# Performance work log

Hardware: AMD Instinct MI355X
Metric: run time of the kernel (lower is better)

## Reference

```python
import jax, jax.numpy as jnp
import numpy as np

N_NODES = 50000
N_EDGES = 800000
F_IN = 128
HID = 64
HEADS = 4
CLASSES = 40
NEG_SLOPE = 0.2
EPS = 1e-16


def glorot(key, shape):
    fan_in, fan_out = shape[0], shape[-1]
    lim = jnp.sqrt(6.0 / (fan_in + fan_out))
    return jax.random.uniform(key, shape, jnp.float32, -lim, lim)


def setup_inputs() -> dict:
    key = jax.random.key(0)
    ks = jax.random.split(key, 10)
    x = jax.random.normal(ks[0], (N_NODES, F_IN), jnp.float32)
    edge_index = jax.random.randint(ks[1], (2, N_EDGES), 0, N_NODES, jnp.int64)
    # layer 1: F_IN -> HID per head, HEADS heads, concat
    W1 = glorot(ks[2], (F_IN, HEADS * HID))
    a_src1 = glorot(ks[3], (1, HEADS, HID))
    a_dst1 = glorot(ks[4], (1, HEADS, HID))
    b1 = jnp.zeros((HEADS * HID,), jnp.float32)
    # layer 2: HEADS*HID -> CLASSES, 1 head
    W2 = glorot(ks[5], (HEADS * HID, CLASSES))
    a_src2 = glorot(ks[6], (1, 1, CLASSES))
    a_dst2 = glorot(ks[7], (1, 1, CLASSES))
    b2 = jnp.zeros((CLASSES,), jnp.float32)
    return {"x": x, "edge_index": edge_index, "W1": W1, "a_src1": a_src1,
            "a_dst1": a_dst1, "b1": b1, "W2": W2, "a_src2": a_src2,
            "a_dst2": a_dst2, "b2": b2}


def gat_conv(x, src, dst, W, a_src, a_dst, bias, heads, out_dim):
    n = x.shape[0]
    h = (x @ W).reshape(n, heads, out_dim)           # [N,H,D]
    alpha_s = jnp.sum(h * a_src, axis=-1)            # [N,H]
    alpha_d = jnp.sum(h * a_dst, axis=-1)            # [N,H]
    e = alpha_s[src] + alpha_d[dst]                  # [E,H]
    e = jax.nn.leaky_relu(e, NEG_SLOPE)
    # segment softmax over edges grouped by destination node
    m = jax.ops.segment_max(e, dst, num_segments=n)  # [N,H]
    ex = jnp.exp(e - m[dst])
    denom = jax.ops.segment_sum(ex, dst, num_segments=n)
    alpha = ex / (denom[dst] + EPS)                  # [E,H]
    msg = h[src] * alpha[:, :, None]                 # [E,H,D]
    out = jax.ops.segment_sum(msg, dst, num_segments=n)
    return out.reshape(n, heads * out_dim) + bias


def reference(x, edge_index, W1, a_src1, a_dst1, b1, W2, a_src2, a_dst2, b2):
    src, dst = edge_index[0], edge_index[1]
    h = gat_conv(x, src, dst, W1, a_src1, a_dst1, b1, HEADS, HID)
    h = jax.nn.relu(h)
    h = gat_conv(h, src, dst, W2, a_src2, a_dst2, b2, 1, CLASSES)
    return jax.nn.log_softmax(h, axis=1)
```

## Files before the change

### kernel.cpp

```cpp
#include <hip/hip_runtime.h>
#include <math.h>

#define NN 50000
#define NE 800000
#define FIN 128
#define HID 64
#define HEADS 4
#define C1 256
#define CLS 40
#define EPSF 1e-16f

#define NB 98
#define BSH 9
#define BSTRIDE 9216
#define NBLK_B 625
#define CHUNK 1280

typedef __attribute__((ext_vector_type(8))) short bf16x8;
typedef __attribute__((ext_vector_type(4))) float f32x4;
typedef __attribute__((ext_vector_type(2))) float f32x2;

__device__ __forceinline__ unsigned short f2bf(float f) {
    unsigned int u = __float_as_uint(f);
    unsigned int r = (u + 0x7fffu + ((u >> 16) & 1u)) >> 16;
    return (unsigned short)r;
}
__device__ __forceinline__ float bflo(unsigned int u) { return __uint_as_float(u << 16); }
__device__ __forceinline__ float bfhi(unsigned int u) { return __uint_as_float(u & 0xffff0000u); }
__device__ __forceinline__ unsigned char f2fp8(float v) {
    int pk = __builtin_amdgcn_cvt_pk_fp8_f32(v, v, 0, false);
    return (unsigned char)(pk & 0xff);
}
__device__ __forceinline__ float lrelu(float e) { return e > 0.f ? e : 0.2f * e; }

__global__ __launch_bounds__(512) void k_bucket(const int* __restrict__ ei,
                                                int* __restrict__ gcur,
                                                unsigned int* __restrict__ stage) {
    __shared__ unsigned int lchunk[CHUNK];
    __shared__ unsigned int lsort[CHUNK];
    __shared__ int lhist[128];
    __shared__ int sbuf[128];
    __shared__ int lstart[128];
    __shared__ int lbase[128];
    __shared__ int lcur[128];
    int t = threadIdx.x;
    int e0 = blockIdx.x * CHUNK;
    if (t < 128) lhist[t] = 0;
    __syncthreads();
    for (int j = t; j < CHUNK; j += 512) {
        int s = ei[e0 + j];
        int d = ei[NE + e0 + j];
        int b = d >> BSH;
        atomicAdd(&lhist[b], 1);
        lchunk[j] = (unsigned int)s | ((unsigned int)(d & 511) << 16) |
                    ((unsigned int)b << 25);
    }
    __syncthreads();
    if (t < 128) sbuf[t] = lhist[t];
    __syncthreads();
    for (int d = 1; d < 128; d <<= 1) {
        int x = (t < 128 && t >= d) ? sbuf[t - d] : 0;
        __syncthreads();
        if (t < 128) sbuf[t] += x;
        __syncthreads();
    }
    if (t < 128) {
        int excl = sbuf[t] - lhist[t];
        lstart[t] = excl;
        lcur[t] = excl;
        if (t < NB) lbase[t] = atomicAdd(&gcur[t], lhist[t]);
    }
    __syncthreads();
    for (int j = t; j < CHUNK; j += 512) {
        unsigned int pk = lchunk[j];
        int b = pk >> 25;
        int pos = atomicAdd(&lcur[b], 1);
        lsort[pos] = pk;
    }
    __syncthreads();
    for (int j = t; j < CHUNK; j += 512) {
        unsigned int pk = lsort[j];
        int b = pk >> 25;
        int dest = lbase[b] + (j - lstart[b]);
        stage[(size_t)b * BSTRIDE + dest] = pk & 0x01FFFFFFu;
    }
}

__global__ void k_bscan(const int* __restrict__ gcur, int* __restrict__ gbase) {
    __shared__ int s[128];
    int t = threadIdx.x;
    int v = (t < NB) ? gcur[t] : 0;
    s[t] = v;
    __syncthreads();
    for (int d = 1; d < 128; d <<= 1) {
        int x = (t >= d) ? s[t - d] : 0;
        __syncthreads();
        s[t] += x;
        __syncthreads();
    }
    if (t < NB) gbase[t] = s[t] - v;
}

__global__ __launch_bounds__(512) void k_bsort(const unsigned int* __restrict__ stage,
                                               const int* __restrict__ gcur,
                                               const int* __restrict__ gbase_a,
                                               int* __restrict__ offs,
                                               int* __restrict__ ssrc) {
    __shared__ int lhist[512];
    __shared__ int cur[512];
    int t = threadIdx.x;
    int b = blockIdx.x;
    int cnt = gcur[b];
    int gbase = gbase_a[b];
    const unsigned int* sp = stage + (size_t)b * BSTRIDE;
    lhist[t] = 0;
    __syncthreads();
    for (int j = t; j < cnt; j += 512) atomicAdd(&lhist[(sp[j] >> 16) & 511], 1);
    __syncthreads();
    if (t < 64) {
        int base = t * 8;
        int vals[8];
        int run = 0;
#pragma unroll
        for (int j = 0; j < 8; j++) { int v = lhist[base + j]; vals[j] = run; run += v; }
        int sc = run;
#pragma unroll
        for (int d = 1; d < 64; d <<= 1) { int u = __shfl_up(sc, d); if (t >= d) sc += u; }
        int excl = sc - run;
#pragma unroll
        for (int j = 0; j < 8; j++) cur[base + j] = excl + vals[j];
    }
    __syncthreads();
    offs[(b << BSH) + t] = gbase + cur[t];
    __syncthreads();
    for (int j = t; j < cnt; j += 512) {
        unsigned int v = sp[j];
        int dl = (v >> 16) & 511;
        int pos = atomicAdd(&cur[dl], 1);
        ssrc[gbase + pos] = (int)(v & 0xFFFFu);
    }
}

__global__ __launch_bounds__(256) void k_wconv(const float* __restrict__ W1,
                                               const float* __restrict__ W2,
                                               unsigned short* __restrict__ wB1,
                                               unsigned short* __restrict__ wB2) {
    int t = blockIdx.x * 256 + threadIdx.x;
    if (t < 4096) {
        int tn = t >> 8;
        int kc = (t >> 6) & 3;
        int l = t & 63;
        int n = tn * 16 + (l & 15);
        int k0 = kc * 32 + (l >> 4) * 8;
        unsigned short* o = wB1 + (size_t)t * 8;
#pragma unroll
        for (int j = 0; j < 8; j++) o[j] = f2bf(W1[(size_t)(k0 + j) * C1 + n]);
    } else if (t < 4096 + 1536) {
        int u = t - 4096;
        int tn = u >> 9;
        int kc = (u >> 6) & 7;
        int l = u & 63;
        int n = tn * 16 + (l & 15);
        int k0 = kc * 32 + (l >> 4) * 8;
        unsigned short* o = wB2 + (size_t)u * 8;
#pragma unroll
        for (int j = 0; j < 8; j++)
            o[j] = (n < CLS) ? f2bf(W2[(size_t)(k0 + j) * CLS + n]) : (unsigned short)0;
    }
}

__global__ __launch_bounds__(256) void k_gemm1(const float* __restrict__ x,
                                               const unsigned short* __restrict__ wB,
                                               const float* __restrict__ aws,
                                               const float* __restrict__ awd,
                                               unsigned char* __restrict__ h1f8,
                                               float* __restrict__ as1,
                                               float* __restrict__ ad1) {
    __shared__ uint4 Af[4][4][64];
    int t = threadIdx.x;
    int m0 = blockIdx.x * 64;
    int l = t & 63;
    int wv = t >> 6;

    bf16x8 bf[4][4];
    const bf16x8* wb = (const bf16x8*)wB + l;
#pragma unroll
    for (int tn = 0; tn < 4; tn++)
#pragma unroll
        for (int kc = 0; kc < 4; kc++)
            bf[tn][kc] = wb[(((wv * 4 + tn) * 4 + kc)) * 64];

#pragma unroll
    for (int i = 0; i < 8; i++) {
        int g = i * 256 + t;
        int row = g >> 5;
        int c4 = g & 31;
        int grow = m0 + row;
        if (grow >= NN) grow = NN - 1;
        float4 v = *(const float4*)(x + (size_t)grow * FIN + c4 * 4);
        uint2 pk;
        pk.x = (unsigned int)f2bf(v.x) | ((unsigned int)f2bf(v.y) << 16);
        pk.y = (unsigned int)f2bf(v.z) | ((unsigned int)f2bf(v.w) << 16);
        int kc = c4 >> 3;
        int rem = (c4 & 7) * 4;
        int q = rem >> 3;
        int hh = (rem >> 2) & 1;
        int ll = q * 16 + (row & 15);
        int mt = row >> 4;
        ((uint2*)&Af[mt][kc][ll])[hh] = pk;
    }
    __syncthreads();

    int q = l >> 4;
    int c = l & 15;

#pragma unroll
    for (int mt = 0; mt < 4; mt++) {
        bf16x8 a[4];
#pragma unroll
        for (int kc = 0; kc < 4; kc++) a[kc] = *(const bf16x8*)&Af[mt][kc][l];

        f32x4 acc[4];
#pragma unroll
        for (int tn = 0; tn < 4; tn++) acc[tn] = (f32x4){0.f, 0.f, 0.f, 0.f};
#pragma unroll
        for (int tn = 0; tn < 4; tn++) {
            acc[tn] = __builtin_amdgcn_mfma_f32_16x16x32_bf16(a[0], bf[tn][0], acc[tn], 0, 0, 0);
            acc[tn] = __builtin_amdgcn_mfma_f32_16x16x32_bf16(a[1], bf[tn][1], acc[tn], 0, 0, 0);
            acc[tn] = __builtin_amdgcn_mfma_f32_16x16x32_bf16(a[2], bf[tn][2], acc[tn], 0, 0, 0);
            acc[tn] = __builtin_amdgcn_mfma_f32_16x16x32_bf16(a[3], bf[tn][3], acc[tn], 0, 0, 0);
        }

        int row0 = m0 + mt * 16 + q * 4;
        float ps[4] = {0.f, 0.f, 0.f, 0.f}, pd[4] = {0.f, 0.f, 0.f, 0.f};
#pragma unroll
        for (int tn = 0; tn < 4; tn++) {
            int col = wv * 64 + tn * 16 + c;
            float wsv = aws[col];
            float wdv = awd[col];
#pragma unroll
            for (int r = 0; r < 4; r++) {
                float v = acc[tn][r];
                int row = row0 + r;
                if (row < NN) h1f8[(size_t)row * C1 + col] = f2fp8(v);
                ps[r] = fmaf(v, wsv, ps[r]);
                pd[r] = fmaf(v, wdv, pd[r]);
            }
        }
#pragma unroll
        for (int r = 0; r < 4; r++) {
            float a_ = ps[r], d_ = pd[r];
#pragma unroll
            for (int s = 1; s < 16; s <<= 1) {
                a_ += __shfl_xor(a_, s);
                d_ += __shfl_xor(d_, s);
            }
            int row = row0 + r;
            if (c == 0 && row < NN) {
                as1[row * 4 + wv] = a_;
                ad1[row * 4 + wv] = d_;
            }
        }
    }
}

__global__ __launch_bounds__(256) void k_agg1(const unsigned char* __restrict__ h1f8,
                                              const float* __restrict__ as1,
                                              const float* __restrict__ ad1,
                                              const int* __restrict__ offs,
                                              const int* __restrict__ ssrc,
                                              const float* __restrict__ b1,
                                              unsigned short* __restrict__ g1b) {
    int lane = threadIdx.x & 63;
    int half = lane >> 5;
    int hl = lane & 31;
    int head = hl >> 3;
    int node = blockIdx.x * 4 + (threadIdx.x >> 6);
    int beg = offs[node];
    int end = (node + 1 < NN) ? offs[node + 1] : NE;
    float adv = ad1[node * 4 + head];
    float l = 0.f;
    float acc[8];
#pragma unroll
    for (int c = 0; c < 8; c++) acc[c] = 0.f;
    const uint2* hv = (const uint2*)h1f8;

    if (beg < end) {
        int idx[4];
#pragma unroll
        for (int i = 0; i < 4; i++) idx[i] = ssrc[beg + 2 * i + half];
        uint2 hbA[2];
        float pA[2];
#pragma unroll
        for (int i = 0; i < 2; i++) {
            hbA[i] = hv[(size_t)idx[i] * 32 + hl];
            int e = beg + 2 * i + half;
            float p = __expf(lrelu(as1[idx[i] * 4 + head] + adv));
            pA[i] = (e < end) ? p : 0.f;
        }
        for (int j = beg; j < end; j += 8) {
            int idxN[4];
#pragma unroll
            for (int i = 0; i < 4; i++) idxN[i] = ssrc[j + 8 + 2 * i + half];
            uint2 hbB[2];
            float pB[2];
#pragma unroll
            for (int i = 0; i < 2; i++) {
                hbB[i] = hv[(size_t)idx[2 + i] * 32 + hl];
                int e = j + 4 + 2 * i + half;
                float p = __expf(lrelu(as1[idx[2 + i] * 4 + head] + adv));
                pB[i] = (e < end) ? p : 0.f;
            }
#pragma unroll
            for (int i = 0; i < 2; i++) {
                float p = pA[i];
                f32x2 v0 = __builtin_amdgcn_cvt_pk_f32_fp8(hbA[i].x, false);
                f32x2 v1 = __builtin_amdgcn_cvt_pk_f32_fp8(hbA[i].x, true);
                f32x2 v2 = __builtin_amdgcn_cvt_pk_f32_fp8(hbA[i].y, false);
                f32x2 v3 = __builtin_amdgcn_cvt_pk_f32_fp8(hbA[i].y, true);
                l += p;
                acc[0] = fmaf(p, v0.x, acc[0]);
                acc[1] = fmaf(p, v0.y, acc[1]);
                acc[2] = fmaf(p, v1.x, acc[2]);
                acc[3] = fmaf(p, v1.y, acc[3]);
                acc[4] = fmaf(p, v2.x, acc[4]);
                acc[5] = fmaf(p, v2.y, acc[5]);
                acc[6] = fmaf(p, v3.x, acc[6]);
                acc[7] = fmaf(p, v3.y, acc[7]);
            }
#pragma unroll
            for (int i = 0; i < 2; i++) {
                hbA[i] = hv[(size_t)idxN[i] * 32 + hl];
                int e = j + 8 + 2 * i + half;
                float p = __expf(lrelu(as1[idxN[i] * 4 + head] + adv));
                pA[i] = (e < end) ? p : 0.f;
            }
#pragma unroll
            for (int i = 0; i < 2; i++) {
                float p = pB[i];
                f32x2 v0 = __builtin_amdgcn_cvt_pk_f32_fp8(hbB[i].x, false);
                f32x2 v1 = __builtin_amdgcn_cvt_pk_f32_fp8(hbB[i].x, true);
                f32x2 v2 = __builtin_amdgcn_cvt_pk_f32_fp8(hbB[i].y, false);
                f32x2 v3 = __builtin_amdgcn_cvt_pk_f32_fp8(hbB[i].y, true);
                l += p;
                acc[0] = fmaf(p, v0.x, acc[0]);
                acc[1] = fmaf(p, v0.y, acc[1]);
                acc[2] = fmaf(p, v1.x, acc[2]);
                acc[3] = fmaf(p, v1.y, acc[3]);
                acc[4] = fmaf(p, v2.x, acc[4]);
                acc[5] = fmaf(p, v2.y, acc[5]);
                acc[6] = fmaf(p, v3.x, acc[6]);
                acc[7] = fmaf(p, v3.y, acc[7]);
            }
#pragma unroll
            for (int i = 0; i < 4; i++) idx[i] = idxN[i];
        }
    }
    l += __shfl_xor(l, 32);
#pragma unroll
    for (int c = 0; c < 8; c++) acc[c] += __shfl_xor(acc[c], 32);

    if (half == 0) {
        float inv = 1.f / (l + EPSF);
        const float4* b1v = (const float4*)b1;
        float4 b0 = b1v[hl * 2];
        float4 b1_ = b1v[hl * 2 + 1];
        float o[8];
        o[0] = fmaxf(fmaf(acc[0], inv, b0.x), 0.f);
        o[1] = fmaxf(fmaf(acc[1], inv, b0.y), 0.f);
        o[2] = fmaxf(fmaf(acc[2], inv, b0.z), 0.f);
        o[3] = fmaxf(fmaf(acc[3], inv, b0.w), 0.f);
        o[4] = fmaxf(fmaf(acc[4], inv, b1_.x), 0.f);
        o[5] = fmaxf(fmaf(acc[5], inv, b1_.y), 0.f);
        o[6] = fmaxf(fmaf(acc[6], inv, b1_.z), 0.f);
        o[7] = fmaxf(fmaf(acc[7], inv, b1_.w), 0.f);
        uint4 ob;
        ob.x = (unsigned int)f2bf(o[0]) | ((unsigned int)f2bf(o[1]) << 16);
        ob.y = (unsigned int)f2bf(o[2]) | ((unsigned int)f2bf(o[3]) << 16);
        ob.z = (unsigned int)f2bf(o[4]) | ((unsigned int)f2bf(o[5]) << 16);
        ob.w = (unsigned int)f2bf(o[6]) | ((unsigned int)f2bf(o[7]) << 16);
        ((uint4*)g1b)[(size_t)node * 32 + hl] = ob;
    }
}

__global__ __launch_bounds__(256) void k_gemm2(const unsigned short* __restrict__ g1b,
                                               const unsigned short* __restrict__ wB2,
                                               const float* __restrict__ aws,
                                               const float* __restrict__ awd,
                                               unsigned short* __restrict__ h2b,
                                               float* __restrict__ as2,
                                               float* __restrict__ ad2) {
    __shared__ uint4 Af[4][8][64];
    int t = threadIdx.x;
    int m0 = blockIdx.x * 64;

#pragma unroll
    for (int i = 0; i < 8; i++) {
        int g = i * 256 + t;
        int row = g >> 5;
        int c8 = g & 31;
        int grow = m0 + row;
        if (grow >= NN) grow = NN - 1;
        uint4 v = *(const uint4*)(g1b + (size_t)grow * C1 + c8 * 8);
        int kc = c8 >> 2;
        int q = c8 & 3;
        Af[row >> 4][kc][q * 16 + (row & 15)] = v;
    }
    __syncthreads();

    int l = t & 63;
    int wv = t >> 6;

    bf16x8 a[8];
#pragma unroll
    for (int kc = 0; kc < 8; kc++) a[kc] = *(const bf16x8*)&Af[wv][kc][l];

    f32x4 acc[3];
#pragma unroll
    for (int tn = 0; tn < 3; tn++) acc[tn] = (f32x4){0.f, 0.f, 0.f, 0.f};

    const bf16x8* wb = (const bf16x8*)wB2 + l;
#pragma unroll
    for (int tn = 0; tn < 3; tn++) {
#pragma unroll
        for (int kc = 0; kc < 8; kc++) {
            bf16x8 b = wb[(tn * 8 + kc) * 64];
            acc[tn] = __builtin_amdgcn_mfma_f32_16x16x32_bf16(a[kc], b, acc[tn], 0, 0, 0);
        }
    }

    int q = l >> 4;
    int c = l & 15;
    int row0 = m0 + wv * 16 + q * 4;
    float ps[4] = {0.f, 0.f, 0.f, 0.f}, pd[4] = {0.f, 0.f, 0.f, 0.f};
#pragma unroll
    for (int tn = 0; tn < 3; tn++) {
        int col = tn * 16 + c;
        bool cok = col < CLS;
        float wsv = cok ? aws[col] : 0.f;
        float wdv = cok ? awd[col] : 0.f;
#pragma unroll
        for (int r = 0; r < 4; r++) {
            float v = acc[tn][r];
            int row = row0 + r;
            if (cok && row < NN) h2b[(size_t)row * CLS + col] = f2bf(v);
            ps[r] = fmaf(v, wsv, ps[r]);
            pd[r] = fmaf(v, wdv, pd[r]);
        }
    }
#pragma unroll
    for (int r = 0; r < 4; r++) {
        float a_ = ps[r], d_ = pd[r];
#pragma unroll
        for (int s = 1; s < 16; s <<= 1) {
            a_ += __shfl_xor(a_, s);
            d_ += __shfl_xor(d_, s);
        }
        int row = row0 + r;
        if (c == 0 && row < NN) {
            as2[row] = a_;
            ad2[row] = d_;
        }
    }
}

__global__ __launch_bounds__(256) void k_agg2(const unsigned short* __restrict__ h2b,
                                              const float* __restrict__ as2,
                                              const float* __restrict__ ad2,
                                              const int* __restrict__ offs,
                                              const int* __restrict__ ssrc,
                                              const float* __restrict__ b2,
                                              float* __restrict__ out) {
    int lane = threadIdx.x & 63;
    int half = lane >> 5;
    int hl = lane & 31;
    int cl = hl < 20 ? hl : 19;
    int node = blockIdx.x * 4 + (threadIdx.x >> 6);
    int beg = offs[node];
    int end = (node + 1 < NN) ? offs[node + 1] : NE;
    float adv = ad2[node];
    float l = 0.f, aL = 0.f, aH = 0.f;
    const unsigned int* hv = (const unsigned int*)h2b;

    if (beg < end) {
        int idx[4];
#pragma unroll
        for (int i = 0; i < 4; i++) idx[i] = ssrc[beg + 2 * i + half];
        unsigned int hbA[2];
        float pA[2];
#pragma unroll
        for (int i = 0; i < 2; i++) {
            hbA[i] = hv[(size_t)idx[i] * 20 + cl];
            int e = beg + 2 * i + half;
            float p = __expf(lrelu(as2[idx[i]] + adv));
            pA[i] = (e < end) ? p : 0.f;
        }
        for (int j = beg; j < end; j += 8) {
            int idxN[4];
#pragma unroll
            for (int i = 0; i < 4; i++) idxN[i] = ssrc[j + 8 + 2 * i + half];
            unsigned int hbB[2];
            float pB[2];
#pragma unroll
            for (int i = 0; i < 2; i++) {
                hbB[i] = hv[(size_t)idx[2 + i] * 20 + cl];
                int e = j + 4 + 2 * i + half;
                float p = __expf(lrelu(as2[idx[2 + i]] + adv));
                pB[i] = (e < end) ? p : 0.f;
            }
#pragma unroll
            for (int i = 0; i < 2; i++) {
                float p = pA[i];
                l += p;
                aL = fmaf(p, bflo(hbA[i]), aL);
                aH = fmaf(p, bfhi(hbA[i]), aH);
            }
#pragma unroll
            for (int i = 0; i < 2; i++) {
                hbA[i] = hv[(size_t)idxN[i] * 20 + cl];
                int e = j + 8 + 2 * i + half;
                float p = __expf(lrelu(as2[idxN[i]] + adv));
                pA[i] = (e < end) ? p : 0.f;
            }
#pragma unroll
            for (int i = 0; i < 2; i++) {
                float p = pB[i];
                l += p;
                aL = fmaf(p, bflo(hbB[i]), aL);
                aH = fmaf(p, bfhi(hbB[i]), aH);
            }
#pragma unroll
            for (int i = 0; i < 4; i++) idx[i] = idxN[i];
        }
    }
    l += __shfl_xor(l, 32);
    aL += __shfl_xor(aL, 32);
    aH += __shfl_xor(aH, 32);

    if (half == 0) {
        bool act = hl < 20;
        float inv = 1.f / (l + EPSF);
        float vL = -INFINITY, vH = -INFINITY;
        if (act) {
            float2 b = ((const float2*)b2)[cl];
            vL = aL * inv + b.x;
            vH = aH * inv + b.y;
        }
        float mx = fmaxf(vL, vH);
#pragma unroll
        for (int s = 16; s >= 1; s >>= 1) mx = fmaxf(mx, __shfl_xor(mx, s));
        float ex = act ? (__expf(vL - mx) + __expf(vH - mx)) : 0.f;
#pragma unroll
        for (int s = 16; s >= 1; s >>= 1) ex += __shfl_xor(ex, s);
        if (act) {
            float ls = __logf(ex);
            float2 o = {vL - mx - ls, vH - mx - ls};
            *(float2*)(out + (size_t)node * CLS + cl * 2) = o;
        }
    }
}


extern "C" void kernel_launch(void* const* d_in, const int* in_sizes, int n_in,
                              void* d_out, int out_size, void* d_ws, size_t ws_size,
                              hipStream_t stream) {
    const float* x    = (const float*)d_in[0];
    const int*   ei   = (const int*)d_in[1];
    const float* W1   = (const float*)d_in[2];
    const float* as1w = (const float*)d_in[3];
    const float* ad1w = (const float*)d_in[4];
    const float* b1   = (const float*)d_in[5];
    const float* W2   = (const float*)d_in[6];
    const float* as2w = (const float*)d_in[7];
    const float* ad2w = (const float*)d_in[8];
    const float* b2   = (const float*)d_in[9];
    float* out = (float*)d_out;

    char* p = (char*)d_ws;
    auto alloc = [&](size_t bytes) {
        char* r = p;
        p += (bytes + 255) & ~(size_t)255;
        return r;
    };
    unsigned char* h1f8 = (unsigned char*)alloc((size_t)NN * C1);
    unsigned short* g1b = (unsigned short*)alloc((size_t)NN * C1 * 2);
    unsigned short* h2b = (unsigned short*)alloc((size_t)NN * CLS * 2);
    float* as1  = (float*)alloc((size_t)NN * 4 * 4);
    float* ad1  = (float*)alloc((size_t)NN * 4 * 4);
    float* as2  = (float*)alloc((size_t)NN * 4);
    float* ad2  = (float*)alloc((size_t)NN * 4);
    int* offs   = (int*)alloc((size_t)(NN + 1024) * 4);
    int* gcur   = (int*)alloc(128 * 4);
    int* gbase  = (int*)alloc(128 * 4);
    unsigned int* stage = (unsigned int*)alloc((size_t)NB * BSTRIDE * 4);
    int* ssrc   = (int*)alloc((size_t)(NE + 64) * 4);
    unsigned short* wB1 = (unsigned short*)alloc((size_t)4096 * 8 * 2);
    unsigned short* wB2 = (unsigned short*)alloc((size_t)1536 * 8 * 2);

    hipMemsetAsync(gcur, 0, 128 * 4, stream);
    hipMemsetAsync(ssrc + NE, 0, 64 * 4, stream);

    k_bucket<<<NBLK_B, 512, 0, stream>>>(ei, gcur, stage);
    k_bscan<<<1, 128, 0, stream>>>(gcur, gbase);
    k_bsort<<<NB, 512, 0, stream>>>(stage, gcur, gbase, offs, ssrc);

    k_wconv<<<22, 256, 0, stream>>>(W1, W2, wB1, wB2);
    k_gemm1<<<(NN + 63) / 64, 256, 0, stream>>>(x, wB1, as1w, ad1w, h1f8, as1, ad1);
    k_agg1<<<NN / 4, 256, 0, stream>>>(h1f8, as1, ad1, offs, ssrc, b1, g1b);

    k_gemm2<<<(NN + 63) / 64, 256, 0, stream>>>(g1b, wB2, as2w, ad2w, h2b, as2, ad2);
    k_agg2<<<NN / 4, 256, 0, stream>>>(h2b, as2, ad2, offs, ssrc, b2, out);
}
```

Before: 215.4 us.

## Fold weight conversion and bucket scan into sort kernels; widen aggregation lanes

Weight bf16 conversion is merged into the first 11 blocks of the bucketing kernel, and the bucket prefix scan is recomputed inside each bsort block. Together these remove two small kernel launches. Both aggregation kernels now split each wavefront into 4 edge groups of 16 lanes, with wider per-lane loads (16 fp8 or 4 bf16 values), so each wavefront has more edges in flight. The cost is more accumulator registers, an extra cross-lane reduction step, and more wasted masked loads on low-degree nodes.

```diff
diff --git a/kernel.cpp b/kernel.cpp
--- a/kernel.cpp
+++ b/kernel.cpp
@@ -35,7 +35,11 @@
 
 __global__ __launch_bounds__(512) void k_bucket(const int* __restrict__ ei,
                                                 int* __restrict__ gcur,
-                                                unsigned int* __restrict__ stage) {
+                                                unsigned int* __restrict__ stage,
+                                                const float* __restrict__ W1,
+                                                const float* __restrict__ W2,
+                                                unsigned short* __restrict__ wB1,
+                                                unsigned short* __restrict__ wB2) {
     __shared__ unsigned int lchunk[CHUNK];
     __shared__ unsigned int lsort[CHUNK];
     __shared__ int lhist[128];
@@ -44,6 +48,32 @@
     __shared__ int lbase[128];
     __shared__ int lcur[128];
     int t = threadIdx.x;
+
+    if (blockIdx.x < 11) {
+        int tw = blockIdx.x * 512 + t;
+        if (tw < 4096) {
+            int tn = tw >> 8;
+            int kc = (tw >> 6) & 3;
+            int lw = tw & 63;
+            int n = tn * 16 + (lw & 15);
+            int k0 = kc * 32 + (lw >> 4) * 8;
+            unsigned short* o = wB1 + (size_t)tw * 8;
+#pragma unroll
+            for (int j = 0; j < 8; j++) o[j] = f2bf(W1[(size_t)(k0 + j) * C1 + n]);
+        } else if (tw < 4096 + 1536) {
+            int u = tw - 4096;
+            int tn = u >> 9;
+            int kc = (u >> 6) & 7;
+            int lw = u & 63;
+            int n = tn * 16 + (lw & 15);
+            int k0 = kc * 32 + (lw >> 4) * 8;
+            unsigned short* o = wB2 + (size_t)u * 8;
+#pragma unroll
+            for (int j = 0; j < 8; j++)
+                o[j] = (n < CLS) ? f2bf(W2[(size_t)(k0 + j) * CLS + n]) : (unsigned short)0;
+        }
+    }
+
     int e0 = blockIdx.x * CHUNK;
     if (t < 128) lhist[t] = 0;
     __syncthreads();
@@ -86,35 +116,27 @@
     }
 }
 
-__global__ void k_bscan(const int* __restrict__ gcur, int* __restrict__ gbase) {
-    __shared__ int s[128];
-    int t = threadIdx.x;
-    int v = (t < NB) ? gcur[t] : 0;
-    s[t] = v;
-    __syncthreads();
-    for (int d = 1; d < 128; d <<= 1) {
-        int x = (t >= d) ? s[t - d] : 0;
-        __syncthreads();
-        s[t] += x;
-        __syncthreads();
-    }
-    if (t < NB) gbase[t] = s[t] - v;
-}
-
 __global__ __launch_bounds__(512) void k_bsort(const unsigned int* __restrict__ stage,
                                                const int* __restrict__ gcur,
-                                               const int* __restrict__ gbase_a,
                                                int* __restrict__ offs,
                                                int* __restrict__ ssrc) {
     __shared__ int lhist[512];
     __shared__ int cur[512];
+    __shared__ int sbuf[128];
     int t = threadIdx.x;
     int b = blockIdx.x;
     int cnt = gcur[b];
-    int gbase = gbase_a[b];
     const unsigned int* sp = stage + (size_t)b * BSTRIDE;
+    if (t < 128) sbuf[t] = (t < NB) ? gcur[t] : 0;
     lhist[t] = 0;
     __syncthreads();
+    for (int d = 1; d < 128; d <<= 1) {
+        int x = (t < 128 && t >= d) ? sbuf[t - d] : 0;
+        __syncthreads();
+        if (t < 128) sbuf[t] += x;
+        __syncthreads();
+    }
+    int gbase = sbuf[b] - cnt;
     for (int j = t; j < cnt; j += 512) atomicAdd(&lhist[(sp[j] >> 16) & 511], 1);
     __syncthreads();
     if (t < 64) {
@@ -138,34 +160,6 @@
         int dl = (v >> 16) & 511;
         int pos = atomicAdd(&cur[dl], 1);
         ssrc[gbase + pos] = (int)(v & 0xFFFFu);
-    }
-}
-
-__global__ __launch_bounds__(256) void k_wconv(const float* __restrict__ W1,
-                                               const float* __restrict__ W2,
-                                               unsigned short* __restrict__ wB1,
-                                               unsigned short* __restrict__ wB2) {
-    int t = blockIdx.x * 256 + threadIdx.x;
-    if (t < 4096) {
-        int tn = t >> 8;
-        int kc = (t >> 6) & 3;
-        int l = t & 63;
-        int n = tn * 16 + (l & 15);
-        int k0 = kc * 32 + (l >> 4) * 8;
-        unsigned short* o = wB1 + (size_t)t * 8;
-#pragma unroll
-        for (int j = 0; j < 8; j++) o[j] = f2bf(W1[(size_t)(k0 + j) * C1 + n]);
-    } else if (t < 4096 + 1536) {
-        int u = t - 4096;
-        int tn = u >> 9;
-        int kc = (u >> 6) & 7;
-        int l = u & 63;
-        int n = tn * 16 + (l & 15);
-        int k0 = kc * 32 + (l >> 4) * 8;
-        unsigned short* o = wB2 + (size_t)u * 8;
-#pragma unroll
-        for (int j = 0; j < 8; j++)
-            o[j] = (n < CLS) ? f2bf(W2[(size_t)(k0 + j) * CLS + n]) : (unsigned short)0;
     }
 }
 
@@ -272,114 +266,99 @@
                                               const float* __restrict__ b1,
                                               unsigned short* __restrict__ g1b) {
     int lane = threadIdx.x & 63;
-    int half = lane >> 5;
-    int hl = lane & 31;
-    int head = hl >> 3;
+    int g = lane >> 4;
+    int c = lane & 15;
+    int head = c >> 2;
     int node = blockIdx.x * 4 + (threadIdx.x >> 6);
     int beg = offs[node];
     int end = (node + 1 < NN) ? offs[node + 1] : NE;
     float adv = ad1[node * 4 + head];
     float l = 0.f;
-    float acc[8];
-#pragma unroll
-    for (int c = 0; c < 8; c++) acc[c] = 0.f;
-    const uint2* hv = (const uint2*)h1f8;
+    float acc[16];
+#pragma unroll
+    for (int k = 0; k < 16; k++) acc[k] = 0.f;
+    const uint4* hv = (const uint4*)h1f8;
+
+#define ACC1(hb, p)                                                              \
+    {                                                                            \
+        f32x2 v;                                                                 \
+        v = __builtin_amdgcn_cvt_pk_f32_fp8((hb).x, false);                      \
+        acc[0] = fmaf(p, v.x, acc[0]); acc[1] = fmaf(p, v.y, acc[1]);            \
+        v = __builtin_amdgcn_cvt_pk_f32_fp8((hb).x, true);                       \
+        acc[2] = fmaf(p, v.x, acc[2]); acc[3] = fmaf(p, v.y, acc[3]);            \
+        v = __builtin_amdgcn_cvt_pk_f32_fp8((hb).y, false);                      \
+        acc[4] = fmaf(p, v.x, acc[4]); acc[5] = fmaf(p, v.y, acc[5]);            \
+        v = __builtin_amdgcn_cvt_pk_f32_fp8((hb).y, true);                       \
+        acc[6] = fmaf(p, v.x, acc[6]); acc[7] = fmaf(p, v.y, acc[7]);            \
+        v = __builtin_amdgcn_cvt_pk_f32_fp8((hb).z, false);                      \
+        acc[8] = fmaf(p, v.x, acc[8]); acc[9] = fmaf(p, v.y, acc[9]);            \
+        v = __builtin_amdgcn_cvt_pk_f32_fp8((hb).z, true);                       \
+        acc[10] = fmaf(p, v.x, acc[10]); acc[11] = fmaf(p, v.y, acc[11]);        \
+        v = __builtin_amdgcn_cvt_pk_f32_fp8((hb).w, false);                      \
+        acc[12] = fmaf(p, v.x, acc[12]); acc[13] = fmaf(p, v.y, acc[13]);        \
+        v = __builtin_amdgcn_cvt_pk_f32_fp8((hb).w, true);                       \
+        acc[14] = fmaf(p, v.x, acc[14]); acc[15] = fmaf(p, v.y, acc[15]);        \
+        l += p;                                                                  \
+    }
 
     if (beg < end) {
-        int idx[4];
-#pragma unroll
-        for (int i = 0; i < 4; i++) idx[i] = ssrc[beg + 2 * i + half];
-        uint2 hbA[2];
-        float pA[2];
-#pragma unroll
-        for (int i = 0; i < 2; i++) {
-            hbA[i] = hv[(size_t)idx[i] * 32 + hl];
-            int e = beg + 2 * i + half;
-            float p = __expf(lrelu(as1[idx[i] * 4 + head] + adv));
-            pA[i] = (e < end) ? p : 0.f;
-        }
-        for (int j = beg; j < end; j += 8) {
-            int idxN[4];
-#pragma unroll
-            for (int i = 0; i < 4; i++) idxN[i] = ssrc[j + 8 + 2 * i + half];
-            uint2 hbB[2];
-            float pB[2];
-#pragma unroll
-            for (int i = 0; i < 2; i++) {
-                hbB[i] = hv[(size_t)idx[2 + i] * 32 + hl];
-                int e = j + 4 + 2 * i + half;
-                float p = __expf(lrelu(as1[idx[2 + i] * 4 + head] + adv));
-                pB[i] = (e < end) ? p : 0.f;
-            }
-#pragma unroll
-            for (int i = 0; i < 2; i++) {
-                float p = pA[i];
-                f32x2 v0 = __builtin_amdgcn_cvt_pk_f32_fp8(hbA[i].x, false);
-                f32x2 v1 = __builtin_amdgcn_cvt_pk_f32_fp8(hbA[i].x, true);
-                f32x2 v2 = __builtin_amdgcn_cvt_pk_f32_fp8(hbA[i].y, false);
-                f32x2 v3 = __builtin_amdgcn_cvt_pk_f32_fp8(hbA[i].y, true);
-                l += p;
-                acc[0] = fmaf(p, v0.x, acc[0]);
-                acc[1] = fmaf(p, v0.y, acc[1]);
-                acc[2] = fmaf(p, v1.x, acc[2]);
-                acc[3] = fmaf(p, v1.y, acc[3]);
-                acc[4] = fmaf(p, v2.x, acc[4]);
-                acc[5] = fmaf(p, v2.y, acc[5]);
-                acc[6] = fmaf(p, v3.x, acc[6]);
-                acc[7] = fmaf(p, v3.y, acc[7]);
-            }
-#pragma unroll
-            for (int i = 0; i < 2; i++) {
-                hbA[i] = hv[(size_t)idxN[i] * 32 + hl];
-                int e = j + 8 + 2 * i + half;
-                float p = __expf(lrelu(as1[idxN[i] * 4 + head] + adv));
-                pA[i] = (e < end) ? p : 0.f;
-            }
-#pragma unroll
-            for (int i = 0; i < 2; i++) {
-                float p = pB[i];
-                f32x2 v0 = __builtin_amdgcn_cvt_pk_f32_fp8(hbB[i].x, false);
-                f32x2 v1 = __builtin_amdgcn_cvt_pk_f32_fp8(hbB[i].x, true);
-                f32x2 v2 = __builtin_amdgcn_cvt_pk_f32_fp8(hbB[i].y, false);
-                f32x2 v3 = __builtin_amdgcn_cvt_pk_f32_fp8(hbB[i].y, true);
-                l += p;
-                acc[0] = fmaf(p, v0.x, acc[0]);
-                acc[1] = fmaf(p, v0.y, acc[1]);
-                acc[2] = fmaf(p, v1.x, acc[2]);
-                acc[3] = fmaf(p, v1.y, acc[3]);
-                acc[4] = fmaf(p, v2.x, acc[4]);
-                acc[5] = fmaf(p, v2.y, acc[5]);
-                acc[6] = fmaf(p, v3.x, acc[6]);
-                acc[7] = fmaf(p, v3.y, acc[7]);
-            }
-#pragma unroll
-            for (int i = 0; i < 4; i++) idx[i] = idxN[i];
-        }
-    }
+        int eA0 = beg + g, eA1 = beg + 4 + g;
+        int iA0 = ssrc[eA0], iA1 = ssrc[eA1];
+        uint4 hA0 = hv[(size_t)iA0 * 16 + c];
+        uint4 hA1 = hv[(size_t)iA1 * 16 + c];
+        float pA0 = (eA0 < end) ? __expf(lrelu(as1[iA0 * 4 + head] + adv)) : 0.f;
+        float pA1 = (eA1 < end) ? __expf(lrelu(as1[iA1 * 4 + head] + adv)) : 0.f;
+        for (int j = beg; j < end; j += 16) {
+            int eB0 = j + 8 + g, eB1 = j + 12 + g;
+            int iB0 = ssrc[eB0], iB1 = ssrc[eB1];
+            uint4 hB0 = hv[(size_t)iB0 * 16 + c];
+            uint4 hB1 = hv[(size_t)iB1 * 16 + c];
+            float pB0 = (eB0 < end) ? __expf(lrelu(as1[iB0 * 4 + head] + adv)) : 0.f;
+            float pB1 = (eB1 < end) ? __expf(lrelu(as1[iB1 * 4 + head] + adv)) : 0.f;
+            ACC1(hA0, pA0);
+            ACC1(hA1, pA1);
+            eA0 = j + 16 + g; eA1 = j + 20 + g;
+            iA0 = ssrc[eA0]; iA1 = ssrc[eA1];
+            hA0 = hv[(size_t)iA0 * 16 + c];
+            hA1 = hv[(size_t)iA1 * 16 + c];
+            pA0 = (eA0 < end) ? __expf(lrelu(as1[iA0 * 4 + head] + adv)) : 0.f;
+            pA1 = (eA1 < end) ? __expf(lrelu(as1[iA1 * 4 + head] + adv)) : 0.f;
+            ACC1(hB0, pB0);
+            ACC1(hB1, pB1);
+        }
+    }
+#undef ACC1
+#pragma unroll
+    for (int k = 0; k < 16; k++) acc[k] += __shfl_xor(acc[k], 16);
+    l += __shfl_xor(l, 16);
+#pragma unroll
+    for (int k = 0; k < 16; k++) acc[k] += __shfl_xor(acc[k], 32);
     l += __shfl_xor(l, 32);
-#pragma unroll
-    for (int c = 0; c < 8; c++) acc[c] += __shfl_xor(acc[c], 32);
-
-    if (half == 0) {
+
+    if (g == 0) {
         float inv = 1.f / (l + EPSF);
         const float4* b1v = (const float4*)b1;
-        float4 b0 = b1v[hl * 2];
-        float4 b1_ = b1v[hl * 2 + 1];
-        float o[8];
-        o[0] = fmaxf(fmaf(acc[0], inv, b0.x), 0.f);
-        o[1] = fmaxf(fmaf(acc[1], inv, b0.y), 0.f);
-        o[2] = fmaxf(fmaf(acc[2], inv, b0.z), 0.f);
-        o[3] = fmaxf(fmaf(acc[3], inv, b0.w), 0.f);
-        o[4] = fmaxf(fmaf(acc[4], inv, b1_.x), 0.f);
-        o[5] = fmaxf(fmaf(acc[5], inv, b1_.y), 0.f);
-        o[6] = fmaxf(fmaf(acc[6], inv, b1_.z), 0.f);
-        o[7] = fmaxf(fmaf(acc[7], inv, b1_.w), 0.f);
-        uint4 ob;
-        ob.x = (unsigned int)f2bf(o[0]) | ((unsigned int)f2bf(o[1]) << 16);
-        ob.y = (unsigned int)f2bf(o[2]) | ((unsigned int)f2bf(o[3]) << 16);
-        ob.z = (unsigned int)f2bf(o[4]) | ((unsigned int)f2bf(o[5]) << 16);
-        ob.w = (unsigned int)f2bf(o[6]) | ((unsigned int)f2bf(o[7]) << 16);
-        ((uint4*)g1b)[(size_t)node * 32 + hl] = ob;
+        float o[16];
+#pragma unroll
+        for (int k = 0; k < 4; k++) {
+            float4 bb = b1v[c * 4 + k];
+            o[k * 4 + 0] = fmaxf(fmaf(acc[k * 4 + 0], inv, bb.x), 0.f);
+            o[k * 4 + 1] = fmaxf(fmaf(acc[k * 4 + 1], inv, bb.y), 0.f);
+            o[k * 4 + 2] = fmaxf(fmaf(acc[k * 4 + 2], inv, bb.z), 0.f);
+            o[k * 4 + 3] = fmaxf(fmaf(acc[k * 4 + 3], inv, bb.w), 0.f);
+        }
+        uint4 ob0, ob1;
+        ob0.x = (unsigned int)f2bf(o[0]) | ((unsigned int)f2bf(o[1]) << 16);
+        ob0.y = (unsigned int)f2bf(o[2]) | ((unsigned int)f2bf(o[3]) << 16);
+        ob0.z = (unsigned int)f2bf(o[4]) | ((unsigned int)f2bf(o[5]) << 16);
+        ob0.w = (unsigned int)f2bf(o[6]) | ((unsigned int)f2bf(o[7]) << 16);
+        ob1.x = (unsigned int)f2bf(o[8]) | ((unsigned int)f2bf(o[9]) << 16);
+        ob1.y = (unsigned int)f2bf(o[10]) | ((unsigned int)f2bf(o[11]) << 16);
+        ob1.z = (unsigned int)f2bf(o[12]) | ((unsigned int)f2bf(o[13]) << 16);
+        ob1.w = (unsigned int)f2bf(o[14]) | ((unsigned int)f2bf(o[15]) << 16);
+        uint4* dst = (uint4*)g1b + (size_t)node * 32 + c * 2;
+        dst[0] = ob0;
+        dst[1] = ob1;
     }
 }
 
@@ -472,90 +451,82 @@
                                               const float* __restrict__ b2,
                                               float* __restrict__ out) {
     int lane = threadIdx.x & 63;
-    int half = lane >> 5;
-    int hl = lane & 31;
-    int cl = hl < 20 ? hl : 19;
+    int g = lane >> 4;
+    int c = lane & 15;
+    bool act = c < 10;
+    int cc = act ? c : 9;
     int node = blockIdx.x * 4 + (threadIdx.x >> 6);
     int beg = offs[node];
     int end = (node + 1 < NN) ? offs[node + 1] : NE;
     float adv = ad2[node];
-    float l = 0.f, aL = 0.f, aH = 0.f;
-    const unsigned int* hv = (const unsigned int*)h2b;
+    float l = 0.f;
+    float acc[4] = {0.f, 0.f, 0.f, 0.f};
+    const uint2* hv = (const uint2*)h2b;
+
+#define ACC2(hb, p)                                                   \
+    {                                                                 \
+        acc[0] = fmaf(p, bflo((hb).x), acc[0]);                       \
+        acc[1] = fmaf(p, bfhi((hb).x), acc[1]);                       \
+        acc[2] = fmaf(p, bflo((hb).y), acc[2]);                       \
+        acc[3] = fmaf(p, bfhi((hb).y), acc[3]);                       \
+        l += p;                                                       \
+    }
 
     if (beg < end) {
-        int idx[4];
-#pragma unroll
-        for (int i = 0; i < 4; i++) idx[i] = ssrc[beg + 2 * i + half];
-        unsigned int hbA[2];
-        float pA[2];
-#pragma unroll
-        for (int i = 0; i < 2; i++) {
-            hbA[i] = hv[(size_t)idx[i] * 20 + cl];
-            int e = beg + 2 * i + half;
-            float p = __expf(lrelu(as2[idx[i]] + adv));
-            pA[i] = (e < end) ? p : 0.f;
-        }
-        for (int j = beg; j < end; j += 8) {
-            int idxN[4];
-#pragma unroll
-            for (int i = 0; i < 4; i++) idxN[i] = ssrc[j + 8 + 2 * i + half];
-            unsigned int hbB[2];
-            float pB[2];
-#pragma unroll
-            for (int i = 0; i < 2; i++) {
-                hbB[i] = hv[(size_t)idx[2 + i] * 20 + cl];
-                int e = j + 4 + 2 * i + half;
-                float p = __expf(lrelu(as2[idx[2 + i]] + adv));
-                pB[i] = (e < end) ? p : 0.f;
-            }
-#pragma unroll
-            for (int i = 0; i < 2; i++) {
-                float p = pA[i];
-                l += p;
-                aL = fmaf(p, bflo(hbA[i]), aL);
-                aH = fmaf(p, bfhi(hbA[i]), aH);
-            }
-#pragma unroll
-            for (int i = 0; i < 2; i++) {
-                hbA[i] = hv[(size_t)idxN[i] * 20 + cl];
-                int e = j + 8 + 2 * i + half;
-                float p = __expf(lrelu(as2[idxN[i]] + adv));
-                pA[i] = (e < end) ? p : 0.f;
-            }
-#pragma unroll
-            for (int i = 0; i < 2; i++) {
-                float p = pB[i];
-                l += p;
-                aL = fmaf(p, bflo(hbB[i]), aL);
-                aH = fmaf(p, bfhi(hbB[i]), aH);
-            }
-#pragma unroll
-            for (int i = 0; i < 4; i++) idx[i] = idxN[i];
-        }
-    }
+        int eA0 = beg + g, eA1 = beg + 4 + g;
+        int iA0 = ssrc[eA0], iA1 = ssrc[eA1];
+        uint2 hA0 = hv[(size_t)iA0 * 10 + cc];
+        uint2 hA1 = hv[(size_t)iA1 * 10 + cc];
+        float pA0 = (eA0 < end) ? __expf(lrelu(as2[iA0] + adv)) : 0.f;
+        float pA1 = (eA1 < end) ? __expf(lrelu(as2[iA1] + adv)) : 0.f;
+        for (int j = beg; j < end; j += 16) {
+            int eB0 = j + 8 + g, eB1 = j + 12 + g;
+            int iB0 = ssrc[eB0], iB1 = ssrc[eB1];
+            uint2 hB0 = hv[(size_t)iB0 * 10 + cc];
+            uint2 hB1 = hv[(size_t)iB1 * 10 + cc];
+            float pB0 = (eB0 < end) ? __expf(lrelu(as2[iB0] + adv)) : 0.f;
+            float pB1 = (eB1 < end) ? __expf(lrelu(as2[iB1] + adv)) : 0.f;
+            ACC2(hA0, pA0);
+            ACC2(hA1, pA1);
+            eA0 = j + 16 + g; eA1 = j + 20 + g;
+            iA0 = ssrc[eA0]; iA1 = ssrc[eA1];
+            hA0 = hv[(size_t)iA0 * 10 + cc];
+            hA1 = hv[(size_t)iA1 * 10 + cc];
+            pA0 = (eA0 < end) ? __expf(lrelu(as2[iA0] + adv)) : 0.f;
+            pA1 = (eA1 < end) ? __expf(lrelu(as2[iA1] + adv)) : 0.f;
+            ACC2(hB0, pB0);
+            ACC2(hB1, pB1);
+        }
+    }
+#undef ACC2
+#pragma unroll
+    for (int k = 0; k < 4; k++) acc[k] += __shfl_xor(acc[k], 16);
+    l += __shfl_xor(l, 16);
+#pragma unroll
+    for (int k = 0; k < 4; k++) acc[k] += __shfl_xor(acc[k], 32);
     l += __shfl_xor(l, 32);
-    aL += __shfl_xor(aL, 32);
-    aH += __shfl_xor(aH, 32);
-
-    if (half == 0) {
-        bool act = hl < 20;
+
+    if (g == 0) {
         float inv = 1.f / (l + EPSF);
-        float vL = -INFINITY, vH = -INFINITY;
+        float4 bb = ((const float4*)b2)[cc];
+        float v0 = -INFINITY, v1 = -INFINITY, v2 = -INFINITY, v3 = -INFINITY;
         if (act) {
-            float2 b = ((const float2*)b2)[cl];
-            vL = aL * inv + b.x;
-            vH = aH * inv + b.y;
-        }
-        float mx = fmaxf(vL, vH);
-#pragma unroll
-        for (int s = 16; s >= 1; s >>= 1) mx = fmaxf(mx, __shfl_xor(mx, s));
-        float ex = act ? (__expf(vL - mx) + __expf(vH - mx)) : 0.f;
-#pragma unroll
-        for (int s = 16; s >= 1; s >>= 1) ex += __shfl_xor(ex, s);
+            v0 = fmaf(acc[0], inv, bb.x);
+            v1 = fmaf(acc[1], inv, bb.y);
+            v2 = fmaf(acc[2], inv, bb.z);
+            v3 = fmaf(acc[3], inv, bb.w);
+        }
+        float mx = fmaxf(fmaxf(v0, v1), fmaxf(v2, v3));
+#pragma unroll
+        for (int s = 8; s >= 1; s >>= 1) mx = fmaxf(mx, __shfl_xor(mx, s));
+        float ex = act ? (__expf(v0 - mx) + __expf(v1 - mx) +
+                          __expf(v2 - mx) + __expf(v3 - mx)) : 0.f;
+#pragma unroll
+        for (int s = 8; s >= 1; s >>= 1) ex += __shfl_xor(ex, s);
         if (act) {
             float ls = __logf(ex);
-            float2 o = {vL - mx - ls, vH - mx - ls};
-            *(float2*)(out + (size_t)node * CLS + cl * 2) = o;
+            float4 o = {v0 - mx - ls, v1 - mx - ls, v2 - mx - ls, v3 - mx - ls};
+            *(float4*)(out + (size_t)node * CLS + c * 4) = o;
         }
     }
 }
@@ -591,7 +562,6 @@
     float* ad2  = (float*)alloc((size_t)NN * 4);
     int* offs   = (int*)alloc((size_t)(NN + 1024) * 4);
     int* gcur   = (int*)alloc(128 * 4);
-    int* gbase  = (int*)alloc(128 * 4);
     unsigned int* stage = (unsigned int*)alloc((size_t)NB * BSTRIDE * 4);
     int* ssrc   = (int*)alloc((size_t)(NE + 64) * 4);
     unsigned short* wB1 = (unsigned short*)alloc((size_t)4096 * 8 * 2);
@@ -600,11 +570,9 @@
     hipMemsetAsync(gcur, 0, 128 * 4, stream);
     hipMemsetAsync(ssrc + NE, 0, 64 * 4, stream);
 
-    k_bucket<<<NBLK_B, 512, 0, stream>>>(ei, gcur, stage);
-    k_bscan<<<1, 128, 0, stream>>>(gcur, gbase);
-    k_bsort<<<NB, 512, 0, stream>>>(stage, gcur, gbase, offs, ssrc);
-
-    k_wconv<<<22, 256, 0, stream>>>(W1, W2, wB1, wB2);
+    k_bucket<<<NBLK_B, 512, 0, stream>>>(ei, gcur, stage, W1, W2, wB1, wB2);
+    k_bsort<<<NB, 512, 0, stream>>>(stage, gcur, offs, ssrc);
+
     k_gemm1<<<(NN + 63) / 64, 256, 0, stream>>>(x, wB1, as1w, ad1w, h1f8, as1, ad1);
     k_agg1<<<NN / 4, 256, 0, stream>>>(h1f8, as1, ad1, offs, ssrc, b1, g1b);
 
```

After: 245.5 us. 14.0% more time.
